# Kernel tuning notes

Measured on AMD Instinct MI355X. Metric: run time of the kernel, lower is better.

The kernel has to match this reference:

```python
import jax, jax.numpy as jnp
import numpy as np

N_NODES = 100000
N_EDGES = 200000
N_GRAPHS = 128
F_NODE, F_EDGE, F_GRAPH = 32, 16, 8
D, D_LIN, D_OUT = 32, 128, 1
MP_TIMES, STEPS = 3, 3


def setup_inputs() -> dict:
    key = jax.random.key(0)
    ks = jax.random.split(key, 26)
    p = lambda i, shape: jax.random.normal(ks[i], shape, dtype=jnp.float32) * 0.1
    return {
        "x": jax.random.normal(ks[0], (N_NODES, F_NODE), dtype=jnp.float32),
        "edge_attr": jax.random.normal(ks[1], (N_EDGES, F_EDGE), dtype=jnp.float32),
        "graph_attr": jax.random.normal(ks[2], (N_GRAPHS, F_GRAPH), dtype=jnp.float32),
        "edge_index": jax.random.randint(ks[3], (2, N_EDGES), 0, N_NODES),
        "batch": jnp.sort(jax.random.randint(ks[4], (N_NODES,), 0, N_GRAPHS)),
        "lin0_w": p(5, (F_NODE, D)), "lin0_b": p(6, (D,)),
        "nn1_w": p(7, (F_EDGE, D_LIN)), "nn1_b": p(8, (D_LIN,)),
        "nn2_w": p(9, (D_LIN, D * D)), "nn2_b": p(10, (D * D,)),
        "root_w": p(11, (D, D)), "conv_b": p(12, (D,)),
        "gru_wih": p(13, (D, 3 * D)), "gru_whh": p(14, (D, 3 * D)),
        "gru_bih": p(15, (3 * D,)), "gru_bhh": p(16, (3 * D,)),
        "lstm_wih": p(17, (2 * D, 4 * D)), "lstm_whh": p(18, (D, 4 * D)),
        "lstm_bih": p(19, (4 * D,)), "lstm_bhh": p(20, (4 * D,)),
        "lin1_w": p(21, (2 * D + F_GRAPH, D)), "lin1_b": p(22, (D,)),
        "lin2_w": p(23, (D, D_OUT)), "lin2_b": p(24, (D_OUT,)),
    }


def reference(x, edge_attr, graph_attr, edge_index, batch,
              lin0_w, lin0_b, nn1_w, nn1_b, nn2_w, nn2_b, root_w, conv_b,
              gru_wih, gru_whh, gru_bih, gru_bhh,
              lstm_wih, lstm_whh, lstm_bih, lstm_bhh,
              lin1_w, lin1_b, lin2_w, lin2_b):
    N = x.shape[0]
    G = graph_attr.shape[0]
    Dd = lin0_w.shape[1]
    src, dst = edge_index[0], edge_index[1]

    out = jax.nn.relu(x @ lin0_w + lin0_b)        # [N, D]
    h = out                                        # GRU hidden state

    # edge-conditioned weight matrices: MLP(edge_attr) -> [E, D, D]
    ew = (jax.nn.relu(edge_attr @ nn1_w + nn1_b) @ nn2_w + nn2_b).reshape(-1, Dd, Dd)
    deg = jnp.maximum(
        jax.ops.segment_sum(jnp.ones(src.shape[0], out.dtype), dst, num_segments=N), 1.0)

    for _ in range(MP_TIMES):
        # NNConv (aggr='mean'): gather-matmul-scatter + root transform
        msg = jnp.einsum('ed,edo->eo', out[src], ew)                 # [E, D]
        agg = jax.ops.segment_sum(msg, dst, num_segments=N) / deg[:, None]
        m = jax.nn.relu(out @ root_w + agg + conv_b)
        # GRU cell (torch gate order r, z, n)
        gi = m @ gru_wih + gru_bih
        gh = h @ gru_whh + gru_bhh
        i_r, i_z, i_n = jnp.split(gi, 3, axis=-1)
        h_r, h_z, h_n = jnp.split(gh, 3, axis=-1)
        r = jax.nn.sigmoid(i_r + h_r)
        z = jax.nn.sigmoid(i_z + h_z)
        n = jnp.tanh(i_n + r * h_n)
        h = (1.0 - z) * n + z * h
        out = h

    # Set2Set attention pooling (LSTM gate order i, f, g, o)
    q_star = jnp.zeros((G, 2 * Dd), out.dtype)
    hs = jnp.zeros((G, Dd), out.dtype)
    cs = jnp.zeros((G, Dd), out.dtype)
    for _ in range(STEPS):
        g = q_star @ lstm_wih + lstm_bih + hs @ lstm_whh + lstm_bhh
        ig, fg, gg, og = jnp.split(g, 4, axis=-1)
        cs = jax.nn.sigmoid(fg) * cs + jax.nn.sigmoid(ig) * jnp.tanh(gg)
        hs = jax.nn.sigmoid(og) * jnp.tanh(cs)                        # query [G, D]
        e = jnp.sum(out * hs[batch], axis=-1)                         # [N]
        emax = jax.ops.segment_max(e, batch, num_segments=G)
        w = jnp.exp(e - emax[batch])
        denom = jax.ops.segment_sum(w, batch, num_segments=G)
        a = w / denom[batch]                                          # segment softmax
        rvec = jax.ops.segment_sum(a[:, None] * out, batch, num_segments=G)
        q_star = jnp.concatenate([hs, rvec], axis=-1)

    z = jax.nn.relu(jnp.concatenate([q_star, graph_attr], axis=1) @ lin1_w + lin1_b)
    return z @ lin2_w + lin2_b
```

## Files before the change

kernel.cpp:

```cpp
#include <hip/hip_runtime.h>
#include <stdint.h>
#include <stddef.h>

#define NND 100000
#define NED 200000
#define NG  128

#define EB 96
#define MSGF_GRID ((NED + EB - 1) / EB)
#define HID_BLOCKS (NED*32/256)
#define LIN0_BLOCKS ((NND + 31) / 32)

typedef unsigned short us4v __attribute__((ext_vector_type(4)));
typedef short bf16x8 __attribute__((ext_vector_type(8)));
typedef float f32x4 __attribute__((ext_vector_type(4)));

__device__ __forceinline__ float bf2f(unsigned short u){
  union{unsigned u; float f;} v; v.u = ((unsigned)u)<<16; return v.f;
}
__device__ __forceinline__ unsigned short f2bf(float f){
  union{float f; unsigned u;} v; v.f = f;
  unsigned r = v.u + 0x7FFFu + ((v.u>>16)&1u);
  return (unsigned short)(r>>16);
}
__device__ __forceinline__ float sigm(float x){ return 1.f/(1.f+__expf(-x)); }
__device__ __forceinline__ float tanh_(float x){ return 2.f/(1.f+__expf(-2.f*x)) - 1.f; }

static const size_t kNeed = 90000000ull;
static void* g_fb = nullptr;
namespace {
struct FB { FB(){ if (hipMalloc(&g_fb, kNeed) != hipSuccess) g_fb = nullptr; } };
static FB g_fb_init;
}


__global__ __launch_bounds__(256) void k_misc(const float* __restrict__ nn2, const float* __restrict__ b2,
                                              unsigned short* __restrict__ Btbl, float* __restrict__ b2tl,
                                              const int* __restrict__ batch,
                                              int* __restrict__ starts, int* __restrict__ counts,
                                              float* __restrict__ deg, float* __restrict__ agg,
                                              const float* __restrict__ ea, const float* __restrict__ w1,
                                              const float* __restrict__ b1, unsigned short* __restrict__ H,
                                              const float* __restrict__ x, const float* __restrict__ w0,
                                              const float* __restrict__ b0, float* __restrict__ cur){
  __shared__ float swh[2048]; __shared__ float sbh[128];
  __shared__ float sw0[1024]; __shared__ float sb0[32];
  __shared__ float sx0[8][32];
  __shared__ int s[129];
  int b = blockIdx.x;
  if (b < 512){
    int t = b*256 + threadIdx.x;
    int j  = t & 7;
    int ln = (t >> 3) & 63;
    int ni = (t >> 9) & 3;
    int ks = (t >> 11) & 3;
    int wc = (t >> 13) & 1;
    int cg = t >> 14;
    int k = ks*32 + (ln >> 4)*8 + j;
    int o = wc*16 + (ln & 15);
    int d = cg*4 + ni;
    Btbl[t] = f2bf(nn2[(k << 10) + d*32 + o]);
    if (t < 1024){
      int ni2 = t & 3, r2 = (t >> 2) & 15, wc2 = (t >> 6) & 1, cg2 = t >> 7;
      int o2 = wc2*16 + r2, d2 = cg2*4 + ni2;
      b2tl[t] = b2[d2*32 + o2];
    }
  } else if (b == 512){
    int g = threadIdx.x;
    if (g < 128){
      int lo = 0, hi = NND;
      while (lo < hi){ int mid = (lo + hi) >> 1; if (batch[mid] < g) lo = mid + 1; else hi = mid; }
      s[g] = lo;
      if (g == 0) s[128] = NND;
    }
    __syncthreads();
    if (g < 128){ starts[g] = s[g]; counts[g] = s[g+1] - s[g]; }
  } else if (b < 1024){
    int idx = (b - 513)*256 + threadIdx.x;
    const int stride = 511*256;
    float4 z; z.x=0.f; z.y=0.f; z.z=0.f; z.w=0.f;
    for (int i = idx; i < (NND*32)/4; i += stride) ((float4*)agg)[i] = z;
    for (int i = idx; i < NND; i += stride) deg[i] = 0.f;
  } else if (b < 1024 + HID_BLOCKS){
    for (int i=threadIdx.x;i<2048;i+=256) swh[i]=w1[i];
    if (threadIdx.x<128) sbh[threadIdx.x]=b1[threadIdx.x];
    __syncthreads();
    int gid = (b - 1024)*256 + threadIdx.x;
    int e = gid >> 5, q = gid & 31;
    float a[16];
    const float4* ap = (const float4*)(ea + (size_t)e*16);
    #pragma unroll
    for (int i=0;i<4;i++){ float4 v=ap[i]; a[4*i]=v.x; a[4*i+1]=v.y; a[4*i+2]=v.z; a[4*i+3]=v.w; }
    float c0=sbh[q*4], c1=sbh[q*4+1], c2=sbh[q*4+2], c3=sbh[q*4+3];
    #pragma unroll
    for (int k=0;k<16;k++){
      float av=a[k]; const float* wr = &swh[k*128 + q*4];
      c0 += av*wr[0]; c1 += av*wr[1]; c2 += av*wr[2]; c3 += av*wr[3];
    }
    us4v o;
    o[0]=f2bf(fmaxf(c0,0.f)); o[1]=f2bf(fmaxf(c1,0.f));
    o[2]=f2bf(fmaxf(c2,0.f)); o[3]=f2bf(fmaxf(c3,0.f));
    *(us4v*)(H + (size_t)e*128 + q*4) = o;
  } else {
    for (int i = threadIdx.x; i < 1024; i += 256) sw0[i] = w0[i];
    if (threadIdx.x < 32) sb0[threadIdx.x] = b0[threadIdx.x];
    __syncthreads();
    int lb = b - (1024 + HID_BLOCKS);
    int ln = threadIdx.x >> 5, j = threadIdx.x & 31;
    for (int it = 0; it < 4; ++it){
      int n = (lb*4 + it)*8 + ln;
      if (n >= NND) return;
      float xj = x[(size_t)n*32 + j];
      sx0[ln][j] = xj;
      float acc = sb0[j];
      #pragma unroll
      for (int d=0; d<32; d++) acc += sx0[ln][d]*sw0[d*32+j];
      cur[(size_t)n*32 + j] = fmaxf(acc, 0.f);
    }
  }
}

__global__ __launch_bounds__(256) void k_deg(const int* __restrict__ dst, float* __restrict__ deg){
  int e = blockIdx.x*256 + threadIdx.x;
  if (e < NED) atomicAdd(&deg[dst[e]], 1.f);
}

__global__ __launch_bounds__(256) void k_msgf(const unsigned short* __restrict__ Hb,
                                              const unsigned short* __restrict__ Btbl,
                                              const float* __restrict__ b2tl,
                                              const float* __restrict__ cur,
                                              const int* __restrict__ src, const int* __restrict__ dst,
                                              float* __restrict__ agg){
  __shared__ char smem[EB*256];
  char* sA = smem;
  float* s_o  = (float*)smem;
  int*   s_dst = (int*)(smem + 13824);
  int tid = threadIdx.x;
  int e0 = blockIdx.x * EB;
  int l = tid & 63, wv = tid >> 6;
  int wr = wv >> 1, wc = wv & 1;
  int r = l & 15, hi = l >> 4;
  const bf16x8* Bfrag = (const bf16x8*)Btbl;
  const float4* b2t4 = (const float4*)b2tl;

  {
    int rr = tid >> 4, c16 = (tid & 15) * 16;
    #pragma unroll
    for (int pass = 0; pass < 6; ++pass){
      int row = pass*16 + rr;
      int ge = e0 + row; if (ge >= NED) ge = NED - 1;
      bf16x8 v = *(const bf16x8*)(Hb + (size_t)ge*128 + (tid&15)*8);
      *(bf16x8*)(sA + row*256 + (c16 ^ ((row&7)<<4))) = v;
    }
  }
  __syncthreads();
  bf16x8 afr[3][4];
  #pragma unroll
  for (int mi=0; mi<3; ++mi){
    int row = wr*48 + mi*16 + r;
    #pragma unroll
    for (int ks=0; ks<4; ++ks){
      int kb = ks*64 + hi*16;
      afr[mi][ks] = *(bf16x8*)(sA + row*256 + (kb ^ ((row&7)<<4)));
    }
  }
  __syncthreads();

  if (tid < EB) s_dst[tid] = dst[min(e0 + tid, NED-1)];
  #pragma unroll
  for (int pass=0; pass<3; ++pass){
    int idx = pass*256 + tid;
    int row = idx >> 3, c4 = (idx & 7)*4;
    int sE = src[min(e0 + row, NED-1)];
    float4 v = *(const float4*)(cur + (size_t)sE*32 + c4);
    *(float4*)(s_o + row*36 + c4) = v;
  }
  __syncthreads();

  float macc[3][4] = {};

  for (int cg = 0; cg < 8; ++cg){
    float4 bzv = b2t4[(cg*2 + wc)*16 + r];
    f32x4 acc[3][4];
    #pragma unroll
    for (int mi=0; mi<3; ++mi)
      #pragma unroll
      for (int ni=0; ni<4; ++ni){
        float bb = (ni==0)?bzv.x:(ni==1)?bzv.y:(ni==2)?bzv.z:bzv.w;
        f32x4 a; a[0]=bb; a[1]=bb; a[2]=bb; a[3]=bb;
        acc[mi][ni] = a;
      }
    #pragma unroll
    for (int ks=0; ks<4; ++ks){
      bf16x8 bfr[4];
      #pragma unroll
      for (int ni=0; ni<4; ++ni)
        bfr[ni] = Bfrag[(size_t)((((cg*2 + wc)*4 + ks)*4 + ni)*64) + l];
      #pragma unroll
      for (int mi=0; mi<3; ++mi)
        #pragma unroll
        for (int ni=0; ni<4; ++ni)
          acc[mi][ni] = __builtin_amdgcn_mfma_f32_16x16x32_bf16(afr[mi][ks], bfr[ni], acc[mi][ni], 0, 0, 0);
    }
    #pragma unroll
    for (int mi=0; mi<3; ++mi)
      #pragma unroll
      for (int q=0; q<4; ++q){
        int e = wr*48 + mi*16 + hi*4 + q;
        float4 od = *(const float4*)(s_o + e*36 + cg*4);
        macc[mi][q] += acc[mi][0][q]*od.x + acc[mi][1][q]*od.y
                     + acc[mi][2][q]*od.z + acc[mi][3][q]*od.w;
      }
  }
  #pragma unroll
  for (int mi=0; mi<3; ++mi)
    #pragma unroll
    for (int q=0; q<4; ++q){
      int e = wr*48 + mi*16 + hi*4 + q;
      if (e0 + e < NED)
        atomicAdd(&agg[(size_t)s_dst[e]*32 + wc*16 + r], macc[mi][q]);
    }
}

__global__ __launch_bounds__(256) void k_gru(float* __restrict__ cur, float* __restrict__ agg,
                                             const float* __restrict__ deg,
                                             const float* __restrict__ root_w, const float* __restrict__ conv_b,
                                             const float* __restrict__ wih, const float* __restrict__ whh,
                                             const float* __restrict__ bih, const float* __restrict__ bhh){
  __shared__ float s_root[1024], s_wih[3072], s_whh[3072], s_cb[32], s_bih[96], s_bhh[96];
  __shared__ float s_c[32][32], s_m[32][32];
  for (int i=threadIdx.x;i<1024;i+=256) s_root[i]=root_w[i];
  for (int i=threadIdx.x;i<3072;i+=256){ s_wih[i]=wih[i]; s_whh[i]=whh[i]; }
  if (threadIdx.x<32) s_cb[threadIdx.x]=conv_b[threadIdx.x];
  if (threadIdx.x<96){ s_bih[threadIdx.x]=bih[threadIdx.x]; s_bhh[threadIdx.x]=bhh[threadIdx.x]; }
  __syncthreads();
  int ln = threadIdx.x >> 5, j = threadIdx.x & 31;
  int base = blockIdx.x * 160;
  for (int g4 = 0; g4 < 5; ++g4){
    float c[4], a[4], idg[4];
    int n[4];
    #pragma unroll
    for (int t=0;t<4;++t){
      n[t] = base + (g4*4 + t)*8 + ln;
      c[t] = cur[(size_t)n[t]*32 + j];
      a[t] = agg[(size_t)n[t]*32 + j];
      agg[(size_t)n[t]*32 + j] = 0.f;
      idg[t] = 1.f / fmaxf(deg[n[t]], 1.f);
      s_c[t*8+ln][j] = c[t];
    }
    float mm[4] = {};
    #pragma unroll 8
    for (int d=0; d<32; ++d){
      float w = s_root[d*32+j];
      #pragma unroll
      for (int t=0;t<4;++t) mm[t] += s_c[t*8+ln][d] * w;
    }
    float m[4];
    #pragma unroll
    for (int t=0;t<4;++t){
      m[t] = fmaxf(mm[t] + a[t]*idg[t] + s_cb[j], 0.f);
      s_m[t*8+ln][j] = m[t];
    }
    float gr[4], gz[4], gn[4], hr[4], hz[4], hh[4];
    #pragma unroll
    for (int t=0;t<4;++t){
      gr[t]=s_bih[j]; gz[t]=s_bih[32+j]; gn[t]=s_bih[64+j];
      hr[t]=s_bhh[j]; hz[t]=s_bhh[32+j]; hh[t]=s_bhh[64+j];
    }
    #pragma unroll 4
    for (int k=0;k<32;++k){
      float w0=s_wih[k*96+j], w1=s_wih[k*96+32+j], w2=s_wih[k*96+64+j];
      float v0=s_whh[k*96+j], v1=s_whh[k*96+32+j], v2=s_whh[k*96+64+j];
      #pragma unroll
      for (int t=0;t<4;++t){
        float mk=s_m[t*8+ln][k], ck=s_c[t*8+ln][k];
        gr[t]+=mk*w0; gz[t]+=mk*w1; gn[t]+=mk*w2;
        hr[t]+=ck*v0; hz[t]+=ck*v1; hh[t]+=ck*v2;
      }
    }
    #pragma unroll
    for (int t=0;t<4;++t){
      float r = sigm(gr[t]+hr[t]);
      float z = sigm(gz[t]+hz[t]);
      float nnv = tanh_(gn[t] + r*hh[t]);
      cur[(size_t)n[t]*32 + j] = (1.f-z)*nnv + z*c[t];
    }
  }
}

__global__ __launch_bounds__(256) void k_s2s(const float* __restrict__ cur,
                                             const int* __restrict__ starts, const int* __restrict__ counts,
                                             const float* __restrict__ ga,
                                             const float* __restrict__ lwih, const float* __restrict__ lwhh,
                                             const float* __restrict__ lbih, const float* __restrict__ lbhh,
                                             const float* __restrict__ w1, const float* __restrict__ b1,
                                             const float* __restrict__ w2, const float* __restrict__ b2,
                                             float* __restrict__ ev, float* __restrict__ out){
  int g = blockIdx.x;
  int s0 = starts[g], cnt = counts[g];
  int tid = threadIdx.x;
  __shared__ float hs[32], cs[32], rv[32], sg[128];
  __shared__ float red[256];
  if (tid < 32){ hs[tid]=0.f; cs[tid]=0.f; rv[tid]=0.f; }
  __syncthreads();
  for (int step=0; step<3; ++step){
    if (tid < 128){
      int j = tid;
      float acc = lbih[j] + lbhh[j];
      #pragma unroll 8
      for (int k=0;k<32;k++){
        acc += hs[k]*(lwih[k*128+j] + lwhh[k*128+j]);
        acc += rv[k]*lwih[(32+k)*128+j];
      }
      sg[j] = acc;
    }
    __syncthreads();
    if (tid < 32){
      int j = tid;
      float cn = sigm(sg[32+j])*cs[j] + sigm(sg[j])*tanh_(sg[64+j]);
      cs[j] = cn;
      hs[j] = sigm(sg[96+j])*tanh_(cn);
    }
    __syncthreads();
    float lmax = -3.4e38f;
    for (int i = tid; i < cnt; i += 256){
      const float4* cp = (const float4*)(cur + (size_t)(s0+i)*32);
      float acc = 0.f;
      #pragma unroll
      for (int q=0;q<8;q++){ float4 v=cp[q]; acc += v.x*hs[q*4]+v.y*hs[q*4+1]+v.z*hs[q*4+2]+v.w*hs[q*4+3]; }
      ev[s0+i] = acc;
      lmax = fmaxf(lmax, acc);
    }
    red[tid] = lmax; __syncthreads();
    #pragma unroll
    for (int st=128; st>0; st>>=1){ if (tid<st) red[tid]=fmaxf(red[tid],red[tid+st]); __syncthreads(); }
    float mx = red[0]; __syncthreads();
    float vec[32];
    #pragma unroll
    for (int k=0;k<32;k++) vec[k]=0.f;
    float lsum = 0.f;
    for (int i = tid; i < cnt; i += 256){
      float w = __expf(ev[s0+i]-mx);
      lsum += w;
      const float4* cp = (const float4*)(cur + (size_t)(s0+i)*32);
      #pragma unroll
      for (int q=0;q<8;q++){ float4 v=cp[q]; vec[q*4]+=w*v.x; vec[q*4+1]+=w*v.y; vec[q*4+2]+=w*v.z; vec[q*4+3]+=w*v.w; }
    }
    red[tid] = lsum; __syncthreads();
    #pragma unroll
    for (int st=128; st>0; st>>=1){ if (tid<st) red[tid]+=red[tid+st]; __syncthreads(); }
    float inv = 1.f/red[0];
    if (tid < 32) rv[tid] = 0.f;
    __syncthreads();
    #pragma unroll
    for (int k=0;k<32;k++){
      float v = vec[k];
      #pragma unroll
      for (int o=32;o>0;o>>=1) v += __shfl_down(v, o, 64);
      if ((tid&63)==0) atomicAdd(&rv[k], v);
    }
    __syncthreads();
    if (tid < 32) rv[tid] *= inv;
    __syncthreads();
  }
  if (tid < 32){
    int j = tid;
    float acc = b1[j];
    #pragma unroll 8
    for (int k=0;k<32;k++) acc += hs[k]*w1[k*32+j];
    #pragma unroll 8
    for (int k=0;k<32;k++) acc += rv[k]*w1[(32+k)*32+j];
    #pragma unroll
    for (int k=0;k<8;k++)  acc += ga[g*8+k]*w1[(64+k)*32+j];
    float r = fmaxf(acc, 0.f)*w2[j];
    #pragma unroll
    for (int o=16;o>0;o>>=1) r += __shfl_down(r, o, 64);
    if (j == 0) out[g] = r + b2[0];
  }
}

extern "C" void kernel_launch(void* const* d_in, const int* in_sizes, int n_in,
                              void* d_out, int out_size, void* d_ws, size_t ws_size,
                              hipStream_t stream){
  (void)in_sizes; (void)n_in; (void)out_size;
  const float* x         = (const float*)d_in[0];
  const float* edge_attr = (const float*)d_in[1];
  const float* graph_attr= (const float*)d_in[2];
  const int*   eidx      = (const int*)d_in[3];
  const int*   batch     = (const int*)d_in[4];
  const float* lin0_w    = (const float*)d_in[5];
  const float* lin0_b    = (const float*)d_in[6];
  const float* nn1_w     = (const float*)d_in[7];
  const float* nn1_b     = (const float*)d_in[8];
  const float* nn2_w     = (const float*)d_in[9];
  const float* nn2_b     = (const float*)d_in[10];
  const float* root_w    = (const float*)d_in[11];
  const float* conv_b    = (const float*)d_in[12];
  const float* gru_wih   = (const float*)d_in[13];
  const float* gru_whh   = (const float*)d_in[14];
  const float* gru_bih   = (const float*)d_in[15];
  const float* gru_bhh   = (const float*)d_in[16];
  const float* lstm_wih  = (const float*)d_in[17];
  const float* lstm_whh  = (const float*)d_in[18];
  const float* lstm_bih  = (const float*)d_in[19];
  const float* lstm_bhh  = (const float*)d_in[20];
  const float* lin1_w    = (const float*)d_in[21];
  const float* lin1_b    = (const float*)d_in[22];
  const float* lin2_w    = (const float*)d_in[23];
  const float* lin2_b    = (const float*)d_in[24];
  const int* src = eidx;
  const int* dst = eidx + NED;

  char* pool = (ws_size >= kNeed) ? (char*)d_ws : (char*)g_fb;
  if (!pool) pool = (char*)d_ws;
  size_t off = 0;
  auto alloc = [&](size_t bytes)->char* {
    char* p = pool + off; off += (bytes + 511) & ~(size_t)511; return p;
  };
  unsigned short* H   = (unsigned short*)alloc((size_t)NED*128*2);
  float* cur  = (float*)alloc((size_t)NND*32*4);
  float* agg  = (float*)alloc((size_t)NND*32*4);
  float* deg  = (float*)alloc((size_t)NND*4);
  float* ev   = (float*)alloc((size_t)NND*4);
  unsigned short* Btbl = (unsigned short*)alloc(1024*128*2);
  float* b2tl = (float*)alloc(1024*4);
  int*   counts = (int*)alloc(512);
  int*   startsb= (int*)alloc(512);

  k_misc<<<1024 + HID_BLOCKS + LIN0_BLOCKS, 256, 0, stream>>>(
      nn2_w, nn2_b, Btbl, b2tl, batch, startsb, counts, deg, agg,
      edge_attr, nn1_w, nn1_b, H, x, lin0_w, lin0_b, cur);
  k_deg<<<(NED+255)/256, 256, 0, stream>>>(dst, deg);

  for (int it=0; it<3; ++it){
    k_msgf<<<MSGF_GRID, 256, 0, stream>>>(H, Btbl, b2tl, cur, src, dst, agg);
    k_gru<<<625, 256, 0, stream>>>(cur, agg, deg, root_w, conv_b,
                                   gru_wih, gru_whh, gru_bih, gru_bhh);
  }
  k_s2s<<<NG, 256, 0, stream>>>(cur, startsb, counts, graph_attr,
                                lstm_wih, lstm_whh, lstm_bih, lstm_bhh,
                                lin1_w, lin1_b, lin2_w, lin2_b, ev, (float*)d_out);
}
```

Baseline: 473.2 us.

## Double edge tile per block in k_msgf to reuse B fragments across two sub-tiles

Raises the edge tile of the fused message kernel from 96 to 192 edges and splits it into two 96-edge sub-tiles. Each column group's B fragments are now loaded from global memory once and reused for both sub-tiles, which halves B traffic per edge and halves the grid size. A fragments are re-read from shared memory inside the column-group loop instead of being kept in registers, and shared memory grows to separate, non-aliased buffers. The cost is more LDS reads, higher register and LDS pressure that may lower occupancy, and fewer blocks in flight.

```diff
diff --git a/kernel.cpp b/kernel.cpp
--- a/kernel.cpp
+++ b/kernel.cpp
@@ -6,7 +6,7 @@
 #define NED 200000
 #define NG  128
 
-#define EB 96
+#define EB 192
 #define MSGF_GRID ((NED + EB - 1) / EB)
 #define HID_BLOCKS (NED*32/256)
 #define LIN0_BLOCKS ((NND + 31) / 32)
@@ -131,10 +131,9 @@
                                               const float* __restrict__ cur,
                                               const int* __restrict__ src, const int* __restrict__ dst,
                                               float* __restrict__ agg){
-  __shared__ char smem[EB*256];
-  char* sA = smem;
-  float* s_o  = (float*)smem;
-  int*   s_dst = (int*)(smem + 13824);
+  __shared__ char sA[EB*256];
+  __shared__ float s_o[EB][36];
+  __shared__ int s_dst[EB];
   int tid = threadIdx.x;
   int e0 = blockIdx.x * EB;
   int l = tid & 63, wv = tid >> 6;
@@ -146,80 +145,83 @@
   {
     int rr = tid >> 4, c16 = (tid & 15) * 16;
     #pragma unroll
-    for (int pass = 0; pass < 6; ++pass){
+    for (int pass = 0; pass < 12; ++pass){
       int row = pass*16 + rr;
       int ge = e0 + row; if (ge >= NED) ge = NED - 1;
       bf16x8 v = *(const bf16x8*)(Hb + (size_t)ge*128 + (tid&15)*8);
       *(bf16x8*)(sA + row*256 + (c16 ^ ((row&7)<<4))) = v;
     }
   }
-  __syncthreads();
-  bf16x8 afr[3][4];
-  #pragma unroll
-  for (int mi=0; mi<3; ++mi){
-    int row = wr*48 + mi*16 + r;
-    #pragma unroll
-    for (int ks=0; ks<4; ++ks){
-      int kb = ks*64 + hi*16;
-      afr[mi][ks] = *(bf16x8*)(sA + row*256 + (kb ^ ((row&7)<<4)));
-    }
-  }
-  __syncthreads();
-
   if (tid < EB) s_dst[tid] = dst[min(e0 + tid, NED-1)];
   #pragma unroll
-  for (int pass=0; pass<3; ++pass){
+  for (int pass=0; pass<6; ++pass){
     int idx = pass*256 + tid;
     int row = idx >> 3, c4 = (idx & 7)*4;
     int sE = src[min(e0 + row, NED-1)];
     float4 v = *(const float4*)(cur + (size_t)sE*32 + c4);
-    *(float4*)(s_o + row*36 + c4) = v;
+    *(float4*)(&s_o[row][c4]) = v;
   }
   __syncthreads();
 
-  float macc[3][4] = {};
+  float macc[2][3][4] = {};
 
   for (int cg = 0; cg < 8; ++cg){
     float4 bzv = b2t4[(cg*2 + wc)*16 + r];
-    f32x4 acc[3][4];
-    #pragma unroll
-    for (int mi=0; mi<3; ++mi)
-      #pragma unroll
-      for (int ni=0; ni<4; ++ni){
-        float bb = (ni==0)?bzv.x:(ni==1)?bzv.y:(ni==2)?bzv.z:bzv.w;
-        f32x4 a; a[0]=bb; a[1]=bb; a[2]=bb; a[3]=bb;
-        acc[mi][ni] = a;
+    bf16x8 bfr[4][4];
+    #pragma unroll
+    for (int ks=0; ks<4; ++ks)
+      #pragma unroll
+      for (int ni=0; ni<4; ++ni)
+        bfr[ks][ni] = Bfrag[(size_t)((((cg*2 + wc)*4 + ks)*4 + ni)*64) + l];
+    #pragma unroll
+    for (int sub=0; sub<2; ++sub){
+      bf16x8 afr[3][4];
+      #pragma unroll
+      for (int mi=0; mi<3; ++mi){
+        int row = sub*96 + wr*48 + mi*16 + r;
+        #pragma unroll
+        for (int ks=0; ks<4; ++ks){
+          int kb = ks*64 + hi*16;
+          afr[mi][ks] = *(bf16x8*)(sA + row*256 + (kb ^ ((row&7)<<4)));
+        }
       }
-    #pragma unroll
-    for (int ks=0; ks<4; ++ks){
-      bf16x8 bfr[4];
-      #pragma unroll
-      for (int ni=0; ni<4; ++ni)
-        bfr[ni] = Bfrag[(size_t)((((cg*2 + wc)*4 + ks)*4 + ni)*64) + l];
+      f32x4 acc[3][4];
       #pragma unroll
       for (int mi=0; mi<3; ++mi)
         #pragma unroll
-        for (int ni=0; ni<4; ++ni)
-          acc[mi][ni] = __builtin_amdgcn_mfma_f32_16x16x32_bf16(afr[mi][ks], bfr[ni], acc[mi][ni], 0, 0, 0);
-    }
+        for (int ni=0; ni<4; ++ni){
+          float bb = (ni==0)?bzv.x:(ni==1)?bzv.y:(ni==2)?bzv.z:bzv.w;
+          f32x4 a; a[0]=bb; a[1]=bb; a[2]=bb; a[3]=bb;
+          acc[mi][ni] = a;
+        }
+      #pragma unroll
+      for (int ks=0; ks<4; ++ks)
+        #pragma unroll
+        for (int mi=0; mi<3; ++mi)
+          #pragma unroll
+          for (int ni=0; ni<4; ++ni)
+            acc[mi][ni] = __builtin_amdgcn_mfma_f32_16x16x32_bf16(afr[mi][ks], bfr[ks][ni], acc[mi][ni], 0, 0, 0);
+      #pragma unroll
+      for (int mi=0; mi<3; ++mi)
+        #pragma unroll
+        for (int q=0; q<4; ++q){
+          int e = sub*96 + wr*48 + mi*16 + hi*4 + q;
+          float4 od = *(const float4*)(&s_o[e][cg*4]);
+          macc[sub][mi][q] += acc[mi][0][q]*od.x + acc[mi][1][q]*od.y
+                            + acc[mi][2][q]*od.z + acc[mi][3][q]*od.w;
+        }
+    }
+  }
+  #pragma unroll
+  for (int sub=0; sub<2; ++sub)
     #pragma unroll
     for (int mi=0; mi<3; ++mi)
       #pragma unroll
       for (int q=0; q<4; ++q){
-        int e = wr*48 + mi*16 + hi*4 + q;
-        float4 od = *(const float4*)(s_o + e*36 + cg*4);
-        macc[mi][q] += acc[mi][0][q]*od.x + acc[mi][1][q]*od.y
-                     + acc[mi][2][q]*od.z + acc[mi][3][q]*od.w;
+        int e = sub*96 + wr*48 + mi*16 + hi*4 + q;
+        if (e0 + e < NED)
+          atomicAdd(&agg[(size_t)s_dst[e]*32 + wc*16 + r], macc[sub][mi][q]);
       }
-  }
-  #pragma unroll
-  for (int mi=0; mi<3; ++mi)
-    #pragma unroll
-    for (int q=0; q<4; ++q){
-      int e = wr*48 + mi*16 + hi*4 + q;
-      if (e0 + e < NED)
-        atomicAdd(&agg[(size_t)s_dst[e]*32 + wc*16 + r], macc[mi][q]);
-    }
 }
 
 __global__ __launch_bounds__(256) void k_gru(float* __restrict__ cur, float* __restrict__ agg,
```

After: 559.6 us. 1.18x slower.
